# Performance work log

Measured on AMD Instinct MI355X. Metric: run time of the kernel, lower is better.

The kernel has to match this reference:

```python
import jax, jax.numpy as jnp
import numpy as np

N, E, H, ATOM, BOND, G, DEPTH = 100000, 400000, 256, 133, 14, 512, 4


def _lin(k, out_dim, in_dim):
    kw, kb = jax.random.split(k)
    s = 1.0 / np.sqrt(in_dim)
    w = jax.random.uniform(kw, (out_dim, in_dim), jnp.float32, -s, s)
    b = jax.random.uniform(kb, (out_dim,), jnp.float32, -s, s)
    return w, b


def setup_inputs() -> dict:
    key = jax.random.key(0)
    ks = jax.random.split(key, 16)
    # paired directed edges: edge 2i and 2i+1 are reverses of each other
    src_half = jax.random.randint(ks[0], (E // 2,), 0, N)
    dst_half = jax.random.randint(ks[1], (E // 2,), 0, N)
    edge_src = jnp.stack([src_half, dst_half], axis=1).reshape(-1)
    edge_dst = jnp.stack([dst_half, src_half], axis=1).reshape(-1)
    b2rev = jnp.arange(E, dtype=jnp.int64) ^ 1
    node_to_graph = jnp.sort(jax.random.randint(ks[2], (N,), 0, G))
    atom_feats = jax.random.normal(ks[3], (N, ATOM), jnp.float32)
    edge_feats = jax.random.normal(ks[4], (E, BOND), jnp.float32)
    edge_weights = jax.random.uniform(ks[5], (E,), jnp.float32)
    Wi, _ = _lin(ks[6], H, ATOM + BOND)  # W_initial, bias=False
    Wm_w, Wm_b = _lin(ks[7], H, H)
    Wn_w, Wn_b = _lin(ks[8], H, ATOM + H)
    nh0_w, nh0_b = _lin(ks[9], H, H)
    nh2_w, nh2_b = _lin(ks[10], ATOM, H)
    eh0_w, eh0_b = _lin(ks[11], H, H)
    eh2_w, eh2_b = _lin(ks[12], BOND, H)
    gh0_w, gh0_b = _lin(ks[13], H, H)
    gh2_w, gh2_b = _lin(ks[14], 1, H)
    return dict(atom_feats=atom_feats, edge_feats=edge_feats, edge_weights=edge_weights,
                Wi=Wi, Wm_w=Wm_w, Wm_b=Wm_b, Wn_w=Wn_w, Wn_b=Wn_b,
                nh0_w=nh0_w, nh0_b=nh0_b, nh2_w=nh2_w, nh2_b=nh2_b,
                eh0_w=eh0_w, eh0_b=eh0_b, eh2_w=eh2_w, eh2_b=eh2_b,
                gh0_w=gh0_w, gh0_b=gh0_b, gh2_w=gh2_w, gh2_b=gh2_b,
                edge_src=edge_src, edge_dst=edge_dst, b2rev=b2rev,
                node_to_graph=node_to_graph, depth=DEPTH, num_graphs=G)


def reference(atom_feats, edge_feats, edge_weights, Wi, Wm_w, Wm_b, Wn_w, Wn_b,
              nh0_w, nh0_b, nh2_w, nh2_b, eh0_w, eh0_b, eh2_w, eh2_b,
              gh0_w, gh0_b, gh2_w, gh2_b,
              edge_src, edge_dst, b2rev, node_to_graph, depth, num_graphs):
    Nn = atom_feats.shape[0]
    valid = b2rev >= 0
    rev_idx = jnp.where(valid, b2rev, 0)
    # initial edge hidden states: [E, H]
    h = jax.nn.relu(jnp.concatenate([atom_feats[edge_src], edge_feats], axis=1) @ Wi.T)
    for _ in range(depth):
        # weighted scatter-add of edge messages onto destination nodes: [N, H]
        M = jax.ops.segment_sum(edge_weights[:, None] * h, edge_dst, num_segments=Nn)
        rev_h = jnp.where(valid[:, None], h[rev_idx], 0.0)
        rev_w = jnp.where(valid, edge_weights[rev_idx], 0.0)
        msg = M[edge_src] - rev_w[:, None] * rev_h  # [E, H]
        h = jax.nn.relu(msg @ Wm_w.T + Wm_b)
    node_agg = jax.ops.segment_sum(edge_weights[:, None] * h, edge_dst, num_segments=Nn)
    node_repr = jax.nn.relu(jnp.concatenate([atom_feats, node_agg], axis=1) @ Wn_w.T + Wn_b)
    graph_embeds = jax.ops.segment_sum(node_repr, node_to_graph, num_segments=num_graphs)
    pred_node = jax.nn.relu(node_repr @ nh0_w.T + nh0_b) @ nh2_w.T + nh2_b
    pred_edge = jax.nn.relu(h @ eh0_w.T + eh0_b) @ eh2_w.T + eh2_b
    pred_graph = (jax.nn.relu(graph_embeds @ gh0_w.T + gh0_b) @ gh2_w.T + gh2_b).squeeze(-1)
    return (pred_node, pred_edge, pred_graph, graph_embeds, node_repr, h)
```

## Files before the change

### kernel.cpp

```cpp
#include <hip/hip_runtime.h>
#include <hip/hip_bf16.h>

#define HDIM 256
#define ATOMF 133
#define BONDF 14
#define DEPTH_HC 4
#define SCAN_CHUNK 1024
#define KWN 416

typedef short bf16x8 __attribute__((ext_vector_type(8)));
typedef float f32x4 __attribute__((ext_vector_type(4)));
typedef unsigned short u16x8 __attribute__((ext_vector_type(8)));
typedef unsigned short u16x4 __attribute__((ext_vector_type(4)));

__device__ inline float bf2f(unsigned short u) {
    unsigned int x = ((unsigned int)u) << 16;
    float f; __builtin_memcpy(&f, &x, 4); return f;
}
__device__ inline unsigned short f2bf(float f) {
    __hip_bfloat16 h = __float2bfloat16(f);
    unsigned short u; __builtin_memcpy(&u, &h, 2); return u;
}

__device__ inline void gload_lds16(const unsigned short* g, unsigned short* lds) {
    __builtin_amdgcn_global_load_lds(
        (const __attribute__((address_space(1))) unsigned int*)g,
        (__attribute__((address_space(3))) unsigned int*)lds, 16, 0, 0);
}

__global__ __launch_bounds__(512) void mfma_gemm_cat(
    const unsigned short* __restrict__ atomb,
    const float* __restrict__ bond,
    const int* __restrict__ src, int E,
    const unsigned short* __restrict__ W,
    unsigned short* __restrict__ Cb)
{
    __shared__ unsigned short As[128 * 32];
    __shared__ unsigned short Bs[256 * 32];
    const int t = threadIdx.x;
    const int w = t >> 6, l = t & 63;
    const int m0 = blockIdx.x * 128;
    const int wr = w >> 2, wc = w & 3;

    f32x4 acc[4][4] = {};

    const int ar = t >> 2;
    const int ac0 = (t & 3) * 8;
    long long e_row = m0 + ar; if (e_row > E - 1) e_row = E - 1;
    const int sn = src[e_row];
    const unsigned short* arow = atomb + (size_t)sn * 160;
    const float* brow = bond + (size_t)e_row * BONDF;

    u16x8 tail = *(const u16x8*)&arow[128 + ac0];
    #pragma unroll
    for (int i = 0; i < 8; ++i) {
        int k = 128 + ac0 + i;
        if (k >= ATOMF && k < ATOMF + BONDF) tail[i] = f2bf(brow[k - ATOMF]);
    }
    u16x8 cur = *(const u16x8*)&arow[ac0];

    const int kcol = (l & 3) * 8;
    const int rowL = (w << 4) + (l >> 2);

    #pragma unroll
    for (int k0 = 0; k0 < 160; k0 += 32) {
        u16x8 nxt = cur;
        if (k0 + 32 < 128) nxt = *(const u16x8*)&arow[k0 + 32 + ac0];
        u16x8 o = (k0 == 128) ? tail : cur;
        *(u16x8*)&As[ar * 32 + ac0] = o;
        gload_lds16(W + (size_t)rowL * 160 + k0 + kcol, Bs + (size_t)w * 512);
        gload_lds16(W + (size_t)(128 + rowL) * 160 + k0 + kcol, Bs + 4096 + (size_t)w * 512);
        __syncthreads();

        const int kq = (l >> 4) * 8;
        const int rbase = (wr << 6) + (l & 15);
        const int cbase = (wc << 6) + (l & 15);
        bf16x8 af[4], bfr[4];
        #pragma unroll
        for (int i = 0; i < 4; ++i) {
            af[i]  = *(const bf16x8*)&As[(rbase + i * 16) * 32 + kq];
            bfr[i] = *(const bf16x8*)&Bs[(cbase + i * 16) * 32 + kq];
        }
        #pragma unroll
        for (int mi = 0; mi < 4; ++mi)
            #pragma unroll
            for (int ni = 0; ni < 4; ++ni)
                acc[mi][ni] = __builtin_amdgcn_mfma_f32_16x16x32_bf16(
                    af[mi], bfr[ni], acc[mi][ni], 0, 0, 0);
        __syncthreads();
        cur = nxt;
    }

    const int ccol = l & 15, crow = (l >> 4) * 4;
    #pragma unroll
    for (int ni = 0; ni < 4; ++ni) {
        int gn = (wc << 6) + ni * 16 + ccol;
        #pragma unroll
        for (int mi = 0; mi < 4; ++mi) {
            #pragma unroll
            for (int j = 0; j < 4; ++j) {
                long long gm = m0 + (wr << 6) + mi * 16 + crow + j;
                if (gm >= E) continue;
                float v = fmaxf(acc[mi][ni][j], 0.0f);
                Cb[(size_t)gm * HDIM + gn] = f2bf(v);
            }
        }
    }
}

__global__ __launch_bounds__(512) void mfma_gemm_msg(
    const unsigned short* __restrict__ Mb,
    const unsigned short* __restrict__ h,
    const float* __restrict__ w,
    const int* __restrict__ src, int E,
    const unsigned short* __restrict__ W,
    const float* __restrict__ bias,
    float* __restrict__ Cf,
    unsigned short* __restrict__ Cb)
{
    __shared__ unsigned short As[128 * 32];
    __shared__ unsigned short Bs[256 * 32];
    const int t = threadIdx.x;
    const int wv = t >> 6, l = t & 63;
    const int m0 = blockIdx.x * 128;
    const int wr = wv >> 2, wc = wv & 3;

    f32x4 acc[4][4] = {};

    const int ar = t >> 2;
    const int ac0 = (t & 3) * 8;
    long long e_row = m0 + ar; if (e_row > E - 1) e_row = E - 1;
    const long long er1 = e_row ^ 1;
    const int sn = src[e_row];
    const float we1 = w[er1];
    const unsigned short* mrow = Mb + (size_t)sn * HDIM;
    const unsigned short* hrow = h + (size_t)er1 * HDIM;

    u16x8 Mv = *(const u16x8*)&mrow[ac0];
    u16x8 hv = *(const u16x8*)&hrow[ac0];

    const int kcol = (l & 3) * 8;
    const int rowL = (wv << 4) + (l >> 2);

    #pragma unroll
    for (int k0 = 0; k0 < 256; k0 += 32) {
        u16x8 Mn = Mv, hn2 = hv;
        if (k0 + 32 < 256) {
            Mn  = *(const u16x8*)&mrow[k0 + 32 + ac0];
            hn2 = *(const u16x8*)&hrow[k0 + 32 + ac0];
        }
        u16x8 o;
        #pragma unroll
        for (int i = 0; i < 8; ++i)
            o[i] = f2bf(bf2f(Mv[i]) - we1 * bf2f(hv[i]));
        *(u16x8*)&As[ar * 32 + ac0] = o;
        gload_lds16(W + (size_t)rowL * 256 + k0 + kcol, Bs + (size_t)wv * 512);
        gload_lds16(W + (size_t)(128 + rowL) * 256 + k0 + kcol, Bs + 4096 + (size_t)wv * 512);
        __syncthreads();

        const int kq = (l >> 4) * 8;
        const int rbase = (wr << 6) + (l & 15);
        const int cbase = (wc << 6) + (l & 15);
        bf16x8 af[4], bfr[4];
        #pragma unroll
        for (int i = 0; i < 4; ++i) {
            af[i]  = *(const bf16x8*)&As[(rbase + i * 16) * 32 + kq];
            bfr[i] = *(const bf16x8*)&Bs[(cbase + i * 16) * 32 + kq];
        }
        #pragma unroll
        for (int mi = 0; mi < 4; ++mi)
            #pragma unroll
            for (int ni = 0; ni < 4; ++ni)
                acc[mi][ni] = __builtin_amdgcn_mfma_f32_16x16x32_bf16(
                    af[mi], bfr[ni], acc[mi][ni], 0, 0, 0);
        __syncthreads();
        Mv = Mn; hv = hn2;
    }

    const int ccol = l & 15, crow = (l >> 4) * 4;
    #pragma unroll
    for (int ni = 0; ni < 4; ++ni) {
        int gn = (wc << 6) + ni * 16 + ccol;
        float bv = bias[gn];
        #pragma unroll
        for (int mi = 0; mi < 4; ++mi) {
            #pragma unroll
            for (int j = 0; j < 4; ++j) {
                long long gm = m0 + (wr << 6) + mi * 16 + crow + j;
                if (gm >= E) continue;
                float v = fmaxf(acc[mi][ni][j] + bv, 0.0f);
                if (Cf) Cf[(size_t)gm * HDIM + gn] = v;
                Cb[(size_t)gm * HDIM + gn] = f2bf(v);
            }
        }
    }
}

__global__ __launch_bounds__(512) void mfma_gemm_catwn(
    const unsigned short* __restrict__ atomb,
    const unsigned short* __restrict__ Mb,
    int N,
    const unsigned short* __restrict__ W,
    const float* __restrict__ bias,
    float* __restrict__ Cf,
    unsigned short* __restrict__ Cb)
{
    __shared__ unsigned short As[128 * 32];
    __shared__ unsigned short Bs[256 * 32];
    const int t = threadIdx.x;
    const int wv = t >> 6, l = t & 63;
    const int m0 = blockIdx.x * 128;
    const int wr = wv >> 2, wc = wv & 3;

    f32x4 acc[4][4] = {};

    const int ar = t >> 2;
    const int ac0 = (t & 3) * 8;
    long long nrow = m0 + ar; if (nrow > N - 1) nrow = N - 1;
    const unsigned short* arow = atomb + (size_t)nrow * 160;
    const unsigned short* mrow = Mb + (size_t)nrow * HDIM;

    u16x8 cur = *(const u16x8*)&arow[ac0];

    const int kcol = (l & 3) * 8;
    const int rowL = (wv << 4) + (l >> 2);

    #pragma unroll
    for (int k0 = 0; k0 < KWN; k0 += 32) {
        u16x8 nxt = cur;
        if (k0 + 32 <= 128)
            nxt = *(const u16x8*)&arow[k0 + 32 + ac0];
        else if (k0 + 32 >= 160 && k0 + 32 <= 384)
            nxt = *(const u16x8*)&mrow[k0 + 32 - 160 + ac0];
        *(u16x8*)&As[ar * 32 + ac0] = cur;
        gload_lds16(W + (size_t)rowL * KWN + k0 + kcol, Bs + (size_t)wv * 512);
        gload_lds16(W + (size_t)(128 + rowL) * KWN + k0 + kcol, Bs + 4096 + (size_t)wv * 512);
        __syncthreads();

        const int kq = (l >> 4) * 8;
        const int rbase = (wr << 6) + (l & 15);
        const int cbase = (wc << 6) + (l & 15);
        bf16x8 af[4], bfr[4];
        #pragma unroll
        for (int i = 0; i < 4; ++i) {
            af[i]  = *(const bf16x8*)&As[(rbase + i * 16) * 32 + kq];
            bfr[i] = *(const bf16x8*)&Bs[(cbase + i * 16) * 32 + kq];
        }
        #pragma unroll
        for (int mi = 0; mi < 4; ++mi)
            #pragma unroll
            for (int ni = 0; ni < 4; ++ni)
                acc[mi][ni] = __builtin_amdgcn_mfma_f32_16x16x32_bf16(
                    af[mi], bfr[ni], acc[mi][ni], 0, 0, 0);
        __syncthreads();
        cur = nxt;
    }

    const int ccol = l & 15, crow = (l >> 4) * 4;
    #pragma unroll
    for (int ni = 0; ni < 4; ++ni) {
        int gn = (wc << 6) + ni * 16 + ccol;
        float bv = bias[gn];
        #pragma unroll
        for (int mi = 0; mi < 4; ++mi) {
            #pragma unroll
            for (int j = 0; j < 4; ++j) {
                long long gm = m0 + (wr << 6) + mi * 16 + crow + j;
                if (gm >= N) continue;
                float v = fmaxf(acc[mi][ni][j] + bv, 0.0f);
                Cf[(size_t)gm * HDIM + gn] = v;
                Cb[(size_t)gm * HDIM + gn] = f2bf(v);
            }
        }
    }
}

__global__ __launch_bounds__(512) void head_fused(
    const unsigned short* __restrict__ A, int Mrows,
    const unsigned short* __restrict__ W,
    const float* __restrict__ b0,
    const unsigned short* __restrict__ W2b,
    const float* __restrict__ b2,
    float* __restrict__ pred, int NOUT2)
{
    __shared__ unsigned short R[128 * 256];
    unsigned short* As = R;
    unsigned short* Bs = R + 128 * 32;
    const int t = threadIdx.x;
    const int w = t >> 6, l = t & 63;
    const int m0 = blockIdx.x * 128;
    const int wr = w >> 2, wc = w & 3;
    const int kq = (l >> 4) * 8;

    f32x4 acc[4][4] = {};
    const int kcol = (l & 3) * 8;
    const int rowL = (w << 4) + (l >> 2);

    #pragma unroll
    for (int k0 = 0; k0 < 256; k0 += 32) {
        long long r0 = m0 + rowL; if (r0 > Mrows - 1) r0 = Mrows - 1;
        gload_lds16(A + (size_t)r0 * 256 + k0 + kcol, As + (size_t)w * 512);
        gload_lds16(W + (size_t)rowL * 256 + k0 + kcol, Bs + (size_t)w * 512);
        gload_lds16(W + (size_t)(128 + rowL) * 256 + k0 + kcol, Bs + 4096 + (size_t)w * 512);
        __syncthreads();

        const int rbase = (wr << 6) + (l & 15);
        const int cbase = (wc << 6) + (l & 15);
        bf16x8 af[4], bfr[4];
        #pragma unroll
        for (int i = 0; i < 4; ++i) {
            af[i]  = *(const bf16x8*)&As[(rbase + i * 16) * 32 + kq];
            bfr[i] = *(const bf16x8*)&Bs[(cbase + i * 16) * 32 + kq];
        }
        #pragma unroll
        for (int mi = 0; mi < 4; ++mi)
            #pragma unroll
            for (int ni = 0; ni < 4; ++ni)
                acc[mi][ni] = __builtin_amdgcn_mfma_f32_16x16x32_bf16(
                    af[mi], bfr[ni], acc[mi][ni], 0, 0, 0);
        __syncthreads();
    }

    const int ccol = l & 15, crow = (l >> 4) * 4;
    #pragma unroll
    for (int ni = 0; ni < 4; ++ni) {
        const int col = (wc << 6) + ni * 16 + ccol;
        const float bv = b0[col];
        #pragma unroll
        for (int mi = 0; mi < 4; ++mi) {
            #pragma unroll
            for (int j = 0; j < 4; ++j) {
                const int rr = (wr << 6) + mi * 16 + crow + j;
                float v = fmaxf(acc[mi][ni][j] + bv, 0.0f);
                size_t byteoff = ((size_t)rr * 512 + (size_t)col * 2) ^ (size_t)((rr & 7) << 4);
                *(unsigned short*)((char*)R + byteoff) = f2bf(v);
            }
        }
    }
    __syncthreads();

    const int erow = (w << 4) + (l & 15);
    const int jrow = l & 15;
    for (int cc = 0; cc * 16 < NOUT2; ++cc) {
        bf16x8 w2b[8];
        #pragma unroll
        for (int ks = 0; ks < 8; ++ks)
            w2b[ks] = *(const bf16x8*)&W2b[(size_t)(cc * 16 + jrow) * 256 + ks * 32 + kq];
        f32x4 acc2 = {};
        #pragma unroll
        for (int ks = 0; ks < 8; ++ks) {
            size_t byteoff = ((size_t)erow * 512 + (size_t)(ks * 64 + kq * 2))
                             ^ (size_t)((erow & 7) << 4);
            bf16x8 af;
            __builtin_memcpy(&af, (char*)R + byteoff, 16);
            acc2 = __builtin_amdgcn_mfma_f32_16x16x32_bf16(af, w2b[ks], acc2, 0, 0, 0);
        }
        const int col = cc * 16 + jrow;
        if (col < NOUT2) {
            #pragma unroll
            for (int j = 0; j < 4; ++j) {
                long long gm = m0 + (w << 4) + (l >> 4) * 4 + j;
                if (gm < Mrows) pred[gm * NOUT2 + col] = acc2[j] + b2[col];
            }
        }
    }
}

__global__ __launch_bounds__(640) void atom_conv(const float* __restrict__ a,
                                                 unsigned short* __restrict__ ab, int N) {
    int n = blockIdx.x * 4 + threadIdx.x / 160;
    int c = threadIdx.x % 160;
    if (n >= N) return;
    ab[(size_t)n * 160 + c] = (c < ATOMF) ? f2bf(a[(size_t)n * ATOMF + c]) : (unsigned short)0;
}

__global__ void pad_all(const float* Wi, const float* Wm, const float* Wn,
                        const float* n0, const float* n2, const float* e0, const float* e2,
                        unsigned short* Wib, unsigned short* Wmb, unsigned short* Wnb,
                        unsigned short* n0b, unsigned short* n2b, unsigned short* e0b,
                        unsigned short* e2b) {
    int wid = blockIdx.x >> 8;
    int r = blockIdx.x & 255;
    if (wid == 2) {
        for (int c = threadIdx.x; c < KWN; c += blockDim.x) {
            float v = 0.0f;
            if (c < ATOMF)      v = Wn[(size_t)r * 389 + c];
            else if (c >= 160)  v = Wn[(size_t)r * 389 + (c - 27)];
            Wnb[(size_t)r * KWN + c] = f2bf(v);
        }
        return;
    }
    const float* S; unsigned short* D; int R, C, Cp;
    switch (wid) {
        case 0: S = Wi; D = Wib; R = 256; C = 147; Cp = 160; break;
        case 1: S = Wm; D = Wmb; R = 256; C = 256; Cp = 256; break;
        case 3: S = n0; D = n0b; R = 256; C = 256; Cp = 256; break;
        case 4: S = n2; D = n2b; R = 133; C = 256; Cp = 256; break;
        case 5: S = e0; D = e0b; R = 256; C = 256; Cp = 256; break;
        default: S = e2; D = e2b; R = 14;  C = 256; Cp = 256; break;
    }
    for (int c = threadIdx.x; c < Cp; c += blockDim.x) {
        float v = (r < R && c < C) ? S[(size_t)r * C + c] : 0.0f;
        D[(size_t)r * Cp + c] = f2bf(v);
    }
}

__global__ void count_dst(const int* __restrict__ dst, int* __restrict__ cnt, int E) {
    int e = blockIdx.x * 256 + threadIdx.x;
    if (e < E) atomicAdd(&cnt[dst[e]], 1);
}

__global__ void scan_reduce(const int* __restrict__ cnt, int* __restrict__ csum, int n) {
    __shared__ int s[256];
    int base = blockIdx.x * SCAN_CHUNK;
    int v = 0;
    for (int i = threadIdx.x; i < SCAN_CHUNK; i += 256) {
        int idx = base + i;
        v += (idx < n) ? cnt[idx] : 0;
    }
    s[threadIdx.x] = v; __syncthreads();
    for (int o = 128; o > 0; o >>= 1) {
        if (threadIdx.x < o) s[threadIdx.x] += s[threadIdx.x + o];
        __syncthreads();
    }
    if (threadIdx.x == 0) csum[blockIdx.x] = s[0];
}

__global__ void scan_sums(const int* __restrict__ csum, int* __restrict__ coff, int nchunks) {
    __shared__ int s[1024];
    int t = threadIdx.x;
    s[t] = (t < nchunks) ? csum[t] : 0;
    __syncthreads();
    for (int o = 1; o < 1024; o <<= 1) {
        int v = (t >= o) ? s[t - o] : 0;
        __syncthreads();
        s[t] += v;
        __syncthreads();
    }
    if (t < nchunks) coff[t] = (t == 0) ? 0 : s[t - 1];
}

__global__ void scan_apply(const int* __restrict__ cnt, const int* __restrict__ coff,
                           int* __restrict__ off, int* __restrict__ cursor, int n) {
    __shared__ int s[256];
    int b = blockIdx.x, t = threadIdx.x;
    if (b == 0 && t == 0) off[0] = 0;
    int base = b * SCAN_CHUNK + t * 4;
    int v[4];
    #pragma unroll
    for (int i = 0; i < 4; ++i) v[i] = (base + i < n) ? cnt[base + i] : 0;
    s[t] = v[0] + v[1] + v[2] + v[3];
    __syncthreads();
    for (int o = 1; o < 256; o <<= 1) {
        int x = (t >= o) ? s[t - o] : 0;
        __syncthreads();
        s[t] += x;
        __syncthreads();
    }
    int run = coff[b] + ((t > 0) ? s[t - 1] : 0);
    #pragma unroll
    for (int i = 0; i < 4; ++i) {
        if (base + i < n) cursor[base + i] = run;
        run += v[i];
        if (base + i < n) off[base + i + 1] = run;
    }
}

__global__ void fill_elist(const int* __restrict__ dst, int* __restrict__ cursor,
                           int* __restrict__ elist, int E) {
    int e = blockIdx.x * 256 + threadIdx.x;
    if (e < E) {
        int p = atomicAdd(&cursor[dst[e]], 1);
        elist[p] = e;
    }
}

__global__ void sort_buckets(const int* __restrict__ off, int* __restrict__ elist, int N) {
    int n = blockIdx.x * 256 + threadIdx.x;
    if (n >= N) return;
    int s = off[n], t = off[n + 1];
    for (int i = s; i < t - 1; ++i) {
        int mn = elist[i], mi = i;
        for (int j = i + 1; j < t; ++j) {
            int v = elist[j];
            if (v < mn) { mn = v; mi = j; }
        }
        if (mi != i) { elist[mi] = elist[i]; elist[i] = mn; }
    }
}

__global__ void gather_M(const unsigned short* __restrict__ h, const float* __restrict__ w,
                         const int* __restrict__ off, const int* __restrict__ elist,
                         unsigned short* __restrict__ Mb, int N) {
    int n = blockIdx.x * 4 + (threadIdx.x >> 6);
    if (n >= N) return;
    int c = (threadIdx.x & 63) * 4;
    int s = off[n], e_ = off[n + 1];
    float4 acc = {0.f, 0.f, 0.f, 0.f};
    for (int i = s; i < e_; i += 4) {
        int m = e_ - i;
        int f[4]; float wf[4]; u16x4 hv[4];
        #pragma unroll
        for (int j = 0; j < 4; ++j) if (j < m) f[j] = elist[i + j];
        #pragma unroll
        for (int j = 0; j < 4; ++j) if (j < m) {
            wf[j] = w[f[j]];
            hv[j] = *(const u16x4*)&h[(size_t)f[j] * HDIM + c];
        }
        #pragma unroll
        for (int j = 0; j < 4; ++j) if (j < m) {
            acc.x += wf[j] * bf2f(hv[j][0]);
            acc.y += wf[j] * bf2f(hv[j][1]);
            acc.z += wf[j] * bf2f(hv[j][2]);
            acc.w += wf[j] * bf2f(hv[j][3]);
        }
    }
    u16x4 o;
    o[0] = f2bf(acc.x); o[1] = f2bf(acc.y); o[2] = f2bf(acc.z); o[3] = f2bf(acc.w);
    *(u16x4*)&Mb[(size_t)n * HDIM + c] = o;
}

__global__ void graph_sum(const float* __restrict__ nr, const int* __restrict__ n2g,
                          float* __restrict__ ge, int N) {
    int g = blockIdx.x, t = threadIdx.x;
    int lo = 0, hi = N;
    while (lo < hi) { int mid = (lo + hi) >> 1; if (n2g[mid] < g) lo = mid + 1; else hi = mid; }
    int start = lo;
    hi = N;
    while (lo < hi) { int mid = (lo + hi) >> 1; if (n2g[mid] < g + 1) lo = mid + 1; else hi = mid; }
    int end = lo;
    float acc = 0.0f;
    for (int n = start; n < end; ++n) acc += nr[(size_t)n * HDIM + t];
    ge[(size_t)g * HDIM + t] = acc;
}

__global__ __launch_bounds__(256) void graph_head(
    const float* __restrict__ ge,
    const float* __restrict__ w0, const float* __restrict__ b0,
    const float* __restrict__ w2, const float* __restrict__ b2,
    float* __restrict__ pred, int G)
{
    int g = blockIdx.x;
    if (g >= G) return;
    __shared__ float xs[256];
    __shared__ float ys[256];
    int t = threadIdx.x;
    xs[t] = ge[(size_t)g * 256 + t];
    __syncthreads();
    float acc = b0[t];
    const float* wr = w0 + (size_t)t * 256;
    #pragma unroll 8
    for (int k = 0; k < 256; ++k) acc = fmaf(wr[k], xs[k], acc);
    ys[t] = fmaxf(acc, 0.0f) * w2[t];
    __syncthreads();
    for (int o = 128; o > 0; o >>= 1) {
        if (t < o) ys[t] += ys[t + o];
        __syncthreads();
    }
    if (t == 0) pred[g] = ys[0] + b2[0];
}

extern "C" void kernel_launch(void* const* d_in, const int* in_sizes, int n_in,
                              void* d_out, int out_size, void* d_ws, size_t ws_size,
                              hipStream_t stream) {
    const float* atom_feats   = (const float*)d_in[0];
    const float* edge_feats   = (const float*)d_in[1];
    const float* edge_weights = (const float*)d_in[2];
    const float* Wi    = (const float*)d_in[3];
    const float* Wm_w  = (const float*)d_in[4];
    const float* Wm_b  = (const float*)d_in[5];
    const float* Wn_w  = (const float*)d_in[6];
    const float* Wn_b  = (const float*)d_in[7];
    const float* nh0_w = (const float*)d_in[8];
    const float* nh0_b = (const float*)d_in[9];
    const float* nh2_w = (const float*)d_in[10];
    const float* nh2_b = (const float*)d_in[11];
    const float* eh0_w = (const float*)d_in[12];
    const float* eh0_b = (const float*)d_in[13];
    const float* eh2_w = (const float*)d_in[14];
    const float* eh2_b = (const float*)d_in[15];
    const float* gh0_w = (const float*)d_in[16];
    const float* gh0_b = (const float*)d_in[17];
    const float* gh2_w = (const float*)d_in[18];
    const float* gh2_b = (const float*)d_in[19];
    const int* edge_src      = (const int*)d_in[20];
    const int* edge_dst      = (const int*)d_in[21];
    const int* node_to_graph = (const int*)d_in[23];

    int N = in_sizes[0] / ATOMF;
    int E = in_sizes[1] / BONDF;
    long long G = ((long long)out_size - (long long)N * (ATOMF + HDIM)
                   - (long long)E * (BONDF + HDIM)) / (1 + HDIM);

    float* out = (float*)d_out;
    float* pred_node = out;
    float* pred_edge = pred_node + (size_t)N * ATOMF;
    float* pred_grph = pred_edge + (size_t)E * BONDF;
    float* gemb      = pred_grph + (size_t)G;
    float* node_repr = gemb + (size_t)G * HDIM;
    float* h_f32     = node_repr + (size_t)N * HDIM;

    unsigned short* hA    = (unsigned short*)d_ws;
    unsigned short* hB    = hA + (size_t)E * HDIM;
    unsigned short* Mb    = hB + (size_t)E * HDIM;
    unsigned short* atomb = Mb + (size_t)N * HDIM;
    unsigned short* Wib   = atomb + (size_t)N * 160;
    unsigned short* Wmb   = Wib + 256 * 160;
    unsigned short* Wnb   = Wmb + 256 * 256;
    unsigned short* nh0b  = Wnb + 256 * KWN;
    unsigned short* nh2b  = nh0b + 256 * 256;
    unsigned short* eh0b  = nh2b + 256 * 256;
    unsigned short* eh2b  = eh0b + 256 * 256;
    int* csr = (int*)(eh2b + 256 * 256);
    int* cnt    = csr;
    int* off    = cnt + N;
    int* cursor = off + N + 1;
    int* elist  = cursor + N;
    int* csum   = elist + E;
    int* coff   = csum + 1024;

    int nchunks = (N + SCAN_CHUNK - 1) / SCAN_CHUNK;

    hipMemsetAsync(cnt, 0, (size_t)N * sizeof(int), stream);
    count_dst<<<(E + 255) / 256, 256, 0, stream>>>(edge_dst, cnt, E);
    scan_reduce<<<nchunks, 256, 0, stream>>>(cnt, csum, N);
    scan_sums<<<1, 1024, 0, stream>>>(csum, coff, nchunks);
    scan_apply<<<nchunks, 256, 0, stream>>>(cnt, coff, off, cursor, N);
    fill_elist<<<(E + 255) / 256, 256, 0, stream>>>(edge_dst, cursor, elist, E);
    sort_buckets<<<(N + 255) / 256, 256, 0, stream>>>(off, elist, N);

    pad_all<<<7 * 256, 256, 0, stream>>>(Wi, Wm_w, Wn_w, nh0_w, nh2_w, eh0_w, eh2_w,
                                         Wib, Wmb, Wnb, nh0b, nh2b, eh0b, eh2b);
    atom_conv<<<(N + 3) / 4, 640, 0, stream>>>(atom_feats, atomb, N);

    mfma_gemm_cat<<<(E + 127) / 128, 512, 0, stream>>>(atomb, edge_feats, edge_src,
                                                       E, Wib, hA);

    int ngrid = (N + 3) / 4;
    unsigned short* hc = hA;
    unsigned short* hn = hB;
    for (int d = 0; d < DEPTH_HC; ++d) {
        gather_M<<<ngrid, 256, 0, stream>>>(hc, edge_weights, off, elist, Mb, N);
        float* cf = (d == DEPTH_HC - 1) ? h_f32 : nullptr;
        mfma_gemm_msg<<<(E + 127) / 128, 512, 0, stream>>>(
            Mb, hc, edge_weights, edge_src, E, Wmb, Wm_b, cf, hn);
        unsigned short* tmp = hc; hc = hn; hn = tmp;
    }

    head_fused<<<(E + 127) / 128, 512, 0, stream>>>(hc, E, eh0b, eh0_b, eh2b, eh2_b,
                                                    pred_edge, BONDF);

    gather_M<<<ngrid, 256, 0, stream>>>(hc, edge_weights, off, elist, Mb, N);
    mfma_gemm_catwn<<<(N + 127) / 128, 512, 0, stream>>>(atomb, Mb, N, Wnb, Wn_b,
                                                         node_repr, hB);

    graph_sum<<<(int)G, HDIM, 0, stream>>>(node_repr, node_to_graph, gemb, N);

    head_fused<<<(N + 127) / 128, 512, 0, stream>>>(hB, N, nh0b, nh0_b, nh2b, nh2_b,
                                                    pred_node, ATOMF);

    graph_head<<<(int)G, 256, 0, stream>>>(gemb, gh0_w, gh0_b, gh2_w, gh2_b,
                                           pred_grph, (int)G);
}
```

Baseline: 2.049 ms.

## Double-buffer LDS tiles in all MFMA GEMM kernels to overlap loads with compute

Converts the four MFMA GEMM kernels (initial concat, message, node Wn, head) from a single LDS buffer with two barriers per K-step to a ping-pong double buffer with one barrier per step. The next K-chunk's A tile and the W tile are issued into the alternate buffer before the MFMAs on the current buffer, so global-to-LDS latency can hide behind compute. This doubles the LDS footprint per block, which may reduce occupancy, and the MFMA step is factored into a shared macro.

```diff
diff --git a/kernel.cpp b/kernel.cpp
--- a/kernel.cpp
+++ b/kernel.cpp
@@ -27,6 +27,25 @@
         (const __attribute__((address_space(1))) unsigned int*)g,
         (__attribute__((address_space(3))) unsigned int*)lds, 16, 0, 0);
 }
+
+#define MFMA_STEP(ASB, BSB)                                                        \
+    {                                                                              \
+        const int kq = (l >> 4) * 8;                                               \
+        const int rbase = (wr << 6) + (l & 15);                                    \
+        const int cbase = (wc << 6) + (l & 15);                                    \
+        bf16x8 af[4], bfr[4];                                                      \
+        _Pragma("unroll")                                                          \
+        for (int i = 0; i < 4; ++i) {                                              \
+            af[i]  = *(const bf16x8*)&(ASB)[(rbase + i * 16) * 32 + kq];           \
+            bfr[i] = *(const bf16x8*)&(BSB)[(cbase + i * 16) * 32 + kq];           \
+        }                                                                          \
+        _Pragma("unroll")                                                          \
+        for (int mi = 0; mi < 4; ++mi)                                             \
+            _Pragma("unroll")                                                      \
+            for (int ni = 0; ni < 4; ++ni)                                         \
+                acc[mi][ni] = __builtin_amdgcn_mfma_f32_16x16x32_bf16(             \
+                    af[mi], bfr[ni], acc[mi][ni], 0, 0, 0);                        \
+    }
 
 __global__ __launch_bounds__(512) void mfma_gemm_cat(
     const unsigned short* __restrict__ atomb,
@@ -35,8 +54,8 @@
     const unsigned short* __restrict__ W,
     unsigned short* __restrict__ Cb)
 {
-    __shared__ unsigned short As[128 * 32];
-    __shared__ unsigned short Bs[256 * 32];
+    __shared__ unsigned short As[2][128 * 32];
+    __shared__ unsigned short Bs[2][256 * 32];
     const int t = threadIdx.x;
     const int w = t >> 6, l = t & 63;
     const int m0 = blockIdx.x * 128;
@@ -57,38 +76,32 @@
         int k = 128 + ac0 + i;
         if (k >= ATOMF && k < ATOMF + BONDF) tail[i] = f2bf(brow[k - ATOMF]);
     }
-    u16x8 cur = *(const u16x8*)&arow[ac0];
 
     const int kcol = (l & 3) * 8;
     const int rowL = (w << 4) + (l >> 2);
 
-    #pragma unroll
-    for (int k0 = 0; k0 < 160; k0 += 32) {
-        u16x8 nxt = cur;
-        if (k0 + 32 < 128) nxt = *(const u16x8*)&arow[k0 + 32 + ac0];
-        u16x8 o = (k0 == 128) ? tail : cur;
-        *(u16x8*)&As[ar * 32 + ac0] = o;
-        gload_lds16(W + (size_t)rowL * 160 + k0 + kcol, Bs + (size_t)w * 512);
-        gload_lds16(W + (size_t)(128 + rowL) * 160 + k0 + kcol, Bs + 4096 + (size_t)w * 512);
-        __syncthreads();
-
-        const int kq = (l >> 4) * 8;
-        const int rbase = (wr << 6) + (l & 15);
-        const int cbase = (wc << 6) + (l & 15);
-        bf16x8 af[4], bfr[4];
-        #pragma unroll
-        for (int i = 0; i < 4; ++i) {
-            af[i]  = *(const bf16x8*)&As[(rbase + i * 16) * 32 + kq];
-            bfr[i] = *(const bf16x8*)&Bs[(cbase + i * 16) * 32 + kq];
-        }
-        #pragma unroll
-        for (int mi = 0; mi < 4; ++mi)
-            #pragma unroll
-            for (int ni = 0; ni < 4; ++ni)
-                acc[mi][ni] = __builtin_amdgcn_mfma_f32_16x16x32_bf16(
-                    af[mi], bfr[ni], acc[mi][ni], 0, 0, 0);
-        __syncthreads();
-        cur = nxt;
+    {
+        u16x8 o = *(const u16x8*)&arow[ac0];
+        *(u16x8*)&As[0][ar * 32 + ac0] = o;
+        gload_lds16(W + (size_t)rowL * 160 + kcol, Bs[0] + (size_t)w * 512);
+        gload_lds16(W + (size_t)(128 + rowL) * 160 + kcol, Bs[0] + 4096 + (size_t)w * 512);
+    }
+    u16x8 regs = *(const u16x8*)&arow[32 + ac0];
+    __syncthreads();
+
+    #pragma unroll
+    for (int c = 0; c < 5; ++c) {
+        const int cb = c & 1, nb = cb ^ 1;
+        if (c + 1 < 5) {
+            u16x8 o = (c + 1 == 4) ? tail : regs;
+            *(u16x8*)&As[nb][ar * 32 + ac0] = o;
+            gload_lds16(W + (size_t)rowL * 160 + (c + 1) * 32 + kcol, Bs[nb] + (size_t)w * 512);
+            gload_lds16(W + (size_t)(128 + rowL) * 160 + (c + 1) * 32 + kcol,
+                        Bs[nb] + 4096 + (size_t)w * 512);
+            if (c + 2 < 4) regs = *(const u16x8*)&arow[(c + 2) * 32 + ac0];
+        }
+        MFMA_STEP(As[cb], Bs[cb]);
+        __syncthreads();
     }
 
     const int ccol = l & 15, crow = (l >> 4) * 4;
@@ -118,8 +131,8 @@
     float* __restrict__ Cf,
     unsigned short* __restrict__ Cb)
 {
-    __shared__ unsigned short As[128 * 32];
-    __shared__ unsigned short Bs[256 * 32];
+    __shared__ unsigned short As[2][128 * 32];
+    __shared__ unsigned short Bs[2][256 * 32];
     const int t = threadIdx.x;
     const int wv = t >> 6, l = t & 63;
     const int m0 = blockIdx.x * 128;
@@ -136,45 +149,41 @@
     const unsigned short* mrow = Mb + (size_t)sn * HDIM;
     const unsigned short* hrow = h + (size_t)er1 * HDIM;
 
-    u16x8 Mv = *(const u16x8*)&mrow[ac0];
-    u16x8 hv = *(const u16x8*)&hrow[ac0];
-
     const int kcol = (l & 3) * 8;
     const int rowL = (wv << 4) + (l >> 2);
 
-    #pragma unroll
-    for (int k0 = 0; k0 < 256; k0 += 32) {
-        u16x8 Mn = Mv, hn2 = hv;
-        if (k0 + 32 < 256) {
-            Mn  = *(const u16x8*)&mrow[k0 + 32 + ac0];
-            hn2 = *(const u16x8*)&hrow[k0 + 32 + ac0];
-        }
+    {
+        u16x8 Mv = *(const u16x8*)&mrow[ac0];
+        u16x8 hv = *(const u16x8*)&hrow[ac0];
         u16x8 o;
         #pragma unroll
-        for (int i = 0; i < 8; ++i)
-            o[i] = f2bf(bf2f(Mv[i]) - we1 * bf2f(hv[i]));
-        *(u16x8*)&As[ar * 32 + ac0] = o;
-        gload_lds16(W + (size_t)rowL * 256 + k0 + kcol, Bs + (size_t)wv * 512);
-        gload_lds16(W + (size_t)(128 + rowL) * 256 + k0 + kcol, Bs + 4096 + (size_t)wv * 512);
-        __syncthreads();
-
-        const int kq = (l >> 4) * 8;
-        const int rbase = (wr << 6) + (l & 15);
-        const int cbase = (wc << 6) + (l & 15);
-        bf16x8 af[4], bfr[4];
-        #pragma unroll
-        for (int i = 0; i < 4; ++i) {
-            af[i]  = *(const bf16x8*)&As[(rbase + i * 16) * 32 + kq];
-            bfr[i] = *(const bf16x8*)&Bs[(cbase + i * 16) * 32 + kq];
-        }
-        #pragma unroll
-        for (int mi = 0; mi < 4; ++mi)
+        for (int i = 0; i < 8; ++i) o[i] = f2bf(bf2f(Mv[i]) - we1 * bf2f(hv[i]));
+        *(u16x8*)&As[0][ar * 32 + ac0] = o;
+        gload_lds16(W + (size_t)rowL * 256 + kcol, Bs[0] + (size_t)wv * 512);
+        gload_lds16(W + (size_t)(128 + rowL) * 256 + kcol, Bs[0] + 4096 + (size_t)wv * 512);
+    }
+    u16x8 Mr = *(const u16x8*)&mrow[32 + ac0];
+    u16x8 hr = *(const u16x8*)&hrow[32 + ac0];
+    __syncthreads();
+
+    #pragma unroll
+    for (int c = 0; c < 8; ++c) {
+        const int cb = c & 1, nb = cb ^ 1;
+        if (c + 1 < 8) {
+            u16x8 o;
             #pragma unroll
-            for (int ni = 0; ni < 4; ++ni)
-                acc[mi][ni] = __builtin_amdgcn_mfma_f32_16x16x32_bf16(
-                    af[mi], bfr[ni], acc[mi][ni], 0, 0, 0);
-        __syncthreads();
-        Mv = Mn; hv = hn2;
+            for (int i = 0; i < 8; ++i) o[i] = f2bf(bf2f(Mr[i]) - we1 * bf2f(hr[i]));
+            *(u16x8*)&As[nb][ar * 32 + ac0] = o;
+            gload_lds16(W + (size_t)rowL * 256 + (c + 1) * 32 + kcol, Bs[nb] + (size_t)wv * 512);
+            gload_lds16(W + (size_t)(128 + rowL) * 256 + (c + 1) * 32 + kcol,
+                        Bs[nb] + 4096 + (size_t)wv * 512);
+            if (c + 2 < 8) {
+                Mr = *(const u16x8*)&mrow[(c + 2) * 32 + ac0];
+                hr = *(const u16x8*)&hrow[(c + 2) * 32 + ac0];
+            }
+        }
+        MFMA_STEP(As[cb], Bs[cb]);
+        __syncthreads();
     }
 
     const int ccol = l & 15, crow = (l >> 4) * 4;
@@ -205,8 +214,8 @@
     float* __restrict__ Cf,
     unsigned short* __restrict__ Cb)
 {
-    __shared__ unsigned short As[128 * 32];
-    __shared__ unsigned short Bs[256 * 32];
+    __shared__ unsigned short As[2][128 * 32];
+    __shared__ unsigned short Bs[2][256 * 32];
     const int t = threadIdx.x;
     const int wv = t >> 6, l = t & 63;
     const int m0 = blockIdx.x * 128;
@@ -220,41 +229,35 @@
     const unsigned short* arow = atomb + (size_t)nrow * 160;
     const unsigned short* mrow = Mb + (size_t)nrow * HDIM;
 
-    u16x8 cur = *(const u16x8*)&arow[ac0];
-
     const int kcol = (l & 3) * 8;
     const int rowL = (wv << 4) + (l >> 2);
 
-    #pragma unroll
-    for (int k0 = 0; k0 < KWN; k0 += 32) {
-        u16x8 nxt = cur;
-        if (k0 + 32 <= 128)
-            nxt = *(const u16x8*)&arow[k0 + 32 + ac0];
-        else if (k0 + 32 >= 160 && k0 + 32 <= 384)
-            nxt = *(const u16x8*)&mrow[k0 + 32 - 160 + ac0];
-        *(u16x8*)&As[ar * 32 + ac0] = cur;
-        gload_lds16(W + (size_t)rowL * KWN + k0 + kcol, Bs + (size_t)wv * 512);
-        gload_lds16(W + (size_t)(128 + rowL) * KWN + k0 + kcol, Bs + 4096 + (size_t)wv * 512);
-        __syncthreads();
-
-        const int kq = (l >> 4) * 8;
-        const int rbase = (wr << 6) + (l & 15);
-        const int cbase = (wc << 6) + (l & 15);
-        bf16x8 af[4], bfr[4];
-        #pragma unroll
-        for (int i = 0; i < 4; ++i) {
-            af[i]  = *(const bf16x8*)&As[(rbase + i * 16) * 32 + kq];
-            bfr[i] = *(const bf16x8*)&Bs[(cbase + i * 16) * 32 + kq];
-        }
-        #pragma unroll
-        for (int mi = 0; mi < 4; ++mi)
-            #pragma unroll
-            for (int ni = 0; ni < 4; ++ni)
-                acc[mi][ni] = __builtin_amdgcn_mfma_f32_16x16x32_bf16(
-                    af[mi], bfr[ni], acc[mi][ni], 0, 0, 0);
-        __syncthreads();
-        cur = nxt;
-    }
+    #define LOADA_WN(c) ((c) < 5 ? *(const u16x8*)&arow[(c) * 32 + ac0] \
+                                 : *(const u16x8*)&mrow[(c) * 32 - 160 + ac0])
+
+    {
+        u16x8 o = LOADA_WN(0);
+        *(u16x8*)&As[0][ar * 32 + ac0] = o;
+        gload_lds16(W + (size_t)rowL * KWN + kcol, Bs[0] + (size_t)wv * 512);
+        gload_lds16(W + (size_t)(128 + rowL) * KWN + kcol, Bs[0] + 4096 + (size_t)wv * 512);
+    }
+    u16x8 regs = LOADA_WN(1);
+    __syncthreads();
+
+    #pragma unroll
+    for (int c = 0; c < 13; ++c) {
+        const int cb = c & 1, nb = cb ^ 1;
+        if (c + 1 < 13) {
+            *(u16x8*)&As[nb][ar * 32 + ac0] = regs;
+            gload_lds16(W + (size_t)rowL * KWN + (c + 1) * 32 + kcol, Bs[nb] + (size_t)wv * 512);
+            gload_lds16(W + (size_t)(128 + rowL) * KWN + (c + 1) * 32 + kcol,
+                        Bs[nb] + 4096 + (size_t)wv * 512);
+            if (c + 2 < 13) regs = LOADA_WN(c + 2);
+        }
+        MFMA_STEP(As[cb], Bs[cb]);
+        __syncthreads();
+    }
+    #undef LOADA_WN
 
     const int ccol = l & 15, crow = (l >> 4) * 4;
     #pragma unroll
@@ -284,8 +287,12 @@
     float* __restrict__ pred, int NOUT2)
 {
     __shared__ unsigned short R[128 * 256];
-    unsigned short* As = R;
-    unsigned short* Bs = R + 128 * 32;
+    unsigned short* As0 = R;
+    unsigned short* As1 = R + 4096;
+    unsigned short* Bs0 = R + 8192;
+    unsigned short* Bs1 = R + 16384;
+    unsigned short* AsB[2] = {As0, As1};
+    unsigned short* BsB[2] = {Bs0, Bs1};
     const int t = threadIdx.x;
     const int w = t >> 6, l = t & 63;
     const int m0 = blockIdx.x * 128;
@@ -295,29 +302,25 @@
     f32x4 acc[4][4] = {};
     const int kcol = (l & 3) * 8;
     const int rowL = (w << 4) + (l >> 2);
-
-    #pragma unroll
-    for (int k0 = 0; k0 < 256; k0 += 32) {
-        long long r0 = m0 + rowL; if (r0 > Mrows - 1) r0 = Mrows - 1;
-        gload_lds16(A + (size_t)r0 * 256 + k0 + kcol, As + (size_t)w * 512);
-        gload_lds16(W + (size_t)rowL * 256 + k0 + kcol, Bs + (size_t)w * 512);
-        gload_lds16(W + (size_t)(128 + rowL) * 256 + k0 + kcol, Bs + 4096 + (size_t)w * 512);
-        __syncthreads();
-
-        const int rbase = (wr << 6) + (l & 15);
-        const int cbase = (wc << 6) + (l & 15);
-        bf16x8 af[4], bfr[4];
-        #pragma unroll
-        for (int i = 0; i < 4; ++i) {
-            af[i]  = *(const bf16x8*)&As[(rbase + i * 16) * 32 + kq];
-            bfr[i] = *(const bf16x8*)&Bs[(cbase + i * 16) * 32 + kq];
-        }
-        #pragma unroll
-        for (int mi = 0; mi < 4; ++mi)
-            #pragma unroll
-            for (int ni = 0; ni < 4; ++ni)
-                acc[mi][ni] = __builtin_amdgcn_mfma_f32_16x16x32_bf16(
-                    af[mi], bfr[ni], acc[mi][ni], 0, 0, 0);
+    long long r0 = m0 + rowL; if (r0 > Mrows - 1) r0 = Mrows - 1;
+
+    {
+        gload_lds16(A + (size_t)r0 * 256 + kcol, As0 + (size_t)w * 512);
+        gload_lds16(W + (size_t)rowL * 256 + kcol, Bs0 + (size_t)w * 512);
+        gload_lds16(W + (size_t)(128 + rowL) * 256 + kcol, Bs0 + 4096 + (size_t)w * 512);
+    }
+    __syncthreads();
+
+    #pragma unroll
+    for (int c = 0; c < 8; ++c) {
+        const int cb = c & 1, nb = cb ^ 1;
+        if (c + 1 < 8) {
+            gload_lds16(A + (size_t)r0 * 256 + (c + 1) * 32 + kcol, AsB[nb] + (size_t)w * 512);
+            gload_lds16(W + (size_t)rowL * 256 + (c + 1) * 32 + kcol, BsB[nb] + (size_t)w * 512);
+            gload_lds16(W + (size_t)(128 + rowL) * 256 + (c + 1) * 32 + kcol,
+                        BsB[nb] + 4096 + (size_t)w * 512);
+        }
+        MFMA_STEP(AsB[cb], BsB[cb]);
         __syncthreads();
     }
 
```

Measured after the change: 1.964 ms. -4.2%, faster.
